# Optimization experiments

Hardware: AMD Instinct MI355X
Metric: run time of the kernel (lower is better)

Reference implementation:

```python
import jax, jax.numpy as jnp
import numpy as np

N_QUBITS = 13
N_ROT = 2
DECOHERENCE_RATE = 0.01
BATCH = 256
DIM = 2 ** N_QUBITS


def setup_inputs() -> dict:
    key = jax.random.key(0)
    k1, k2, k3, k4 = jax.random.split(key, 4)
    return {
        "x": jax.random.normal(k1, (BATCH, 128), dtype=jnp.float32),
        "rx_params": jax.random.normal(k2, (N_QUBITS, N_ROT), dtype=jnp.float32),
        "ry_params": jax.random.normal(k3, (N_QUBITS, N_ROT), dtype=jnp.float32),
        "rz_params": jax.random.normal(k4, (N_QUBITS, N_ROT), dtype=jnp.float32),
    }


def _rx_mat(a):
    c = jnp.cos(a / 2).astype(jnp.complex64)
    s = jnp.sin(a / 2).astype(jnp.complex64)
    mi = jnp.complex64(-1j)
    return jnp.stack([jnp.stack([c, mi * s]), jnp.stack([mi * s, c])])


def _ry_mat(a):
    c = jnp.cos(a / 2).astype(jnp.complex64)
    s = jnp.sin(a / 2).astype(jnp.complex64)
    return jnp.stack([jnp.stack([c, -s]), jnp.stack([s, c])])


def _rz_mat(a):
    e = jnp.exp(jnp.complex64(-1j) * a.astype(jnp.complex64) / 2)
    z = jnp.zeros((), jnp.complex64)
    return jnp.stack([jnp.stack([e, z]), jnp.stack([z, jnp.conj(e)])])


def _apply_axis(state, params, mat_fn):
    # Original torch code ignores the qubit index: every gate acts on the
    # even/odd interleaved pairs of the flat statevector. It also has a view
    # aliasing bug: the odd update reads the ALREADY-UPDATED even amplitudes.
    B = state.shape[0]
    def step(s, angle):
        m = mat_fn(angle)
        p = s.reshape(B, -1, 2)  # [B, DIM/2, 2] (even, odd) pairs
        e, o = p[..., 0], p[..., 1]
        e_new = m[0, 0] * e + m[0, 1] * o
        o_new = m[1, 0] * e_new + m[1, 1] * o  # replicates in-place aliasing bug
        return jnp.stack([e_new, o_new], axis=-1).reshape(B, -1), None
    # params iterated qubit-major, rotation-minor, matching the nested loops
    state, _ = jax.lax.scan(step, state, params.reshape(-1))
    return state


def reference(x, rx_params, ry_params, rz_params):
    B = x.shape[0]
    state = jnp.zeros((B, DIM), dtype=jnp.complex64).at[:, 0].set(1.0)
    state = _apply_axis(state, rx_params, _rx_mat)
    state = _apply_axis(state, ry_params, _ry_mat)
    state = _apply_axis(state, rz_params, _rz_mat)
    # decoherence noise: complex normal (re/im each var 1/2), matching torch.randn_like on complex64
    noise = jax.random.normal(jax.random.key(42), (B, DIM), dtype=jnp.complex64) * DECOHERENCE_RATE
    state = state + noise
    state = state / jnp.linalg.norm(state, axis=-1, keepdims=True)
    return jnp.abs(state)
```

## Files before the change

kernel.cpp:

```cpp
#include <hip/hip_runtime.h>


#define NBATCH 256
#define NDIM   8192u

__host__ __device__ __forceinline__ unsigned rotl32(unsigned v, unsigned d) {
  return (v << d) | (v >> (32u - d));
}

__host__ __device__ inline void tf2x32(unsigned k0, unsigned k1,
                                       unsigned x0, unsigned x1,
                                       unsigned& o0, unsigned& o1) {
  const unsigned k2 = k0 ^ k1 ^ 0x1BD11BDAu;
  x0 += k0; x1 += k1;
#define TF_R(r) { x0 += x1; x1 = rotl32(x1, r); x1 ^= x0; }
  TF_R(13u) TF_R(15u) TF_R(26u) TF_R(6u)
  x0 += k1; x1 += k2 + 1u;
  TF_R(17u) TF_R(29u) TF_R(16u) TF_R(24u)
  x0 += k2; x1 += k0 + 2u;
  TF_R(13u) TF_R(15u) TF_R(26u) TF_R(6u)
  x0 += k0; x1 += k1 + 3u;
  TF_R(17u) TF_R(29u) TF_R(16u) TF_R(24u)
  x0 += k1; x1 += k2 + 4u;
  TF_R(13u) TF_R(15u) TF_R(26u) TF_R(6u)
  x0 += k2; x1 += k0 + 5u;
#undef TF_R
  o0 = x0; o1 = x1;
}

__device__ __forceinline__ float bits_to_u(unsigned bits) {
  float f = __uint_as_float((bits >> 9) | 0x3f800000u) - 1.0f;
  const float LO = -0.99999994f;
  return fmaxf(LO, fmaf(f, 2.0f, LO));
}

__device__ __forceinline__ float erfinv_f(float x) {
  float w = -__logf(fmaf(-x, x, 1.0f));
  float p;
  if (w < 5.0f) {
    w -= 2.5f;
    p = 2.81022636e-08f;
    p = fmaf(p, w, 3.43273939e-07f);
    p = fmaf(p, w, -3.5233877e-06f);
    p = fmaf(p, w, -4.39150654e-06f);
    p = fmaf(p, w, 0.00021858087f);
    p = fmaf(p, w, -0.00125372503f);
    p = fmaf(p, w, -0.00417768164f);
    p = fmaf(p, w, 0.246640727f);
    p = fmaf(p, w, 1.50140941f);
  } else {
    w = sqrtf(w) - 3.0f;
    p = -0.000200214257f;
    p = fmaf(p, w, 0.000100950558f);
    p = fmaf(p, w, 0.00134934322f);
    p = fmaf(p, w, -0.00367342844f);
    p = fmaf(p, w, 0.00573950773f);
    p = fmaf(p, w, -0.0076224613f);
    p = fmaf(p, w, 0.00943887047f);
    p = fmaf(p, w, 1.00167406f);
    p = fmaf(p, w, 2.83297682f);
  }
  return p * x;
}

__device__ __forceinline__ float2 cmul(float2 a, float2 b) {
  return make_float2(a.x * b.x - a.y * b.y, a.x * b.y + a.y * b.x);
}
__device__ __forceinline__ float2 cadd(float2 a, float2 b) {
  return make_float2(a.x + b.x, a.y + b.y);
}

__device__ __forceinline__ void eff_gate(int g, const float* rx, const float* ry,
                                         const float* rz, float2& G00, float2& G01,
                                         float2& G10, float2& G11) {
  if (g >= 78) {
    G00 = make_float2(1.f, 0.f); G01 = make_float2(0.f, 0.f);
    G10 = make_float2(0.f, 0.f); G11 = make_float2(1.f, 0.f);
    return;
  }
  int axis = (g >= 52) ? 2 : ((g >= 26) ? 1 : 0);
  int w = g - axis * 26;
  float a = ((axis == 0) ? rx[w] : (axis == 1) ? ry[w] : rz[w]) * 0.5f;
  float s, c;
  sincosf(a, &s, &c);
  float2 m00, m01, m10, m11;
  if (axis == 0) {
    m00 = make_float2(c, 0.f); m01 = make_float2(0.f, -s);
    m10 = make_float2(0.f, -s); m11 = make_float2(c, 0.f);
  } else if (axis == 1) {
    m00 = make_float2(c, 0.f); m01 = make_float2(-s, 0.f);
    m10 = make_float2(s, 0.f); m11 = make_float2(c, 0.f);
  } else {
    m00 = make_float2(c, -s); m01 = make_float2(0.f, 0.f);
    m10 = make_float2(0.f, 0.f); m11 = make_float2(c, s);
  }
  G00 = m00; G01 = m01;
  G10 = cmul(m10, m00);
  G11 = cadd(cmul(m10, m01), m11);
}

__global__ __launch_bounds__(1024) void fused_kernel(
    const float* __restrict__ rx, const float* __restrict__ ry,
    const float* __restrict__ rz, float* __restrict__ out,
    unsigned kr0, unsigned kr1, unsigned ki0, unsigned ki1) {
  const int b = blockIdx.x;
  const int t = threadIdx.x;
  const unsigned base = (unsigned)b * NDIM;

  float T00r = 0.f, T00i = 0.f, T10r = 0.f, T10i = 0.f;
  if (t < 64) {
    float2 A00, A01, A10, A11, B00, B01, B10, B11;
    eff_gate(2 * t, rx, ry, rz, A00, A01, A10, A11);
    eff_gate(2 * t + 1, rx, ry, rz, B00, B01, B10, B11);
    float2 P00 = cadd(cmul(B00, A00), cmul(B01, A10));
    float2 P01 = cadd(cmul(B00, A01), cmul(B01, A11));
    float2 P10 = cadd(cmul(B10, A00), cmul(B11, A10));
    float2 P11 = cadd(cmul(B10, A01), cmul(B11, A11));
#pragma unroll
    for (int s = 1; s < 64; s <<= 1) {
      float2 Q00, Q01, Q10, Q11;
      Q00.x = __shfl(P00.x, t + s); Q00.y = __shfl(P00.y, t + s);
      Q01.x = __shfl(P01.x, t + s); Q01.y = __shfl(P01.y, t + s);
      Q10.x = __shfl(P10.x, t + s); Q10.y = __shfl(P10.y, t + s);
      Q11.x = __shfl(P11.x, t + s); Q11.y = __shfl(P11.y, t + s);
      if (t + s < 64) {
        float2 R00 = cadd(cmul(Q00, P00), cmul(Q01, P10));
        float2 R01 = cadd(cmul(Q00, P01), cmul(Q01, P11));
        float2 R10 = cadd(cmul(Q10, P00), cmul(Q11, P10));
        float2 R11 = cadd(cmul(Q10, P01), cmul(Q11, P11));
        P00 = R00; P01 = R01; P10 = R10; P11 = R11;
      }
    }
    T00r = P00.x; T00i = P00.y; T10r = P10.x; T10i = P10.y;
  }

  float re[8], im[8];
#pragma unroll
  for (int k = 0; k < 8; ++k) {
    unsigned j = base + (unsigned)t * 8u + (unsigned)k;
    unsigned y0, y1;
    tf2x32(kr0, kr1, 0u, j, y0, y1);
    re[k] = erfinv_f(bits_to_u(y0 ^ y1)) * 0.01f;
    tf2x32(ki0, ki1, 0u, j, y0, y1);
    im[k] = erfinv_f(bits_to_u(y0 ^ y1)) * 0.01f;
  }
  if (t == 0) {
    re[0] += T00r; im[0] += T00i;
    re[1] += T10r; im[1] += T10i;
  }

  float sumsq = 0.0f;
  float a[8];
#pragma unroll
  for (int k = 0; k < 8; ++k) {
    float s2 = fmaf(re[k], re[k], im[k] * im[k]);
    sumsq += s2;
    a[k] = sqrtf(s2);
  }

#pragma unroll
  for (int off = 32; off; off >>= 1) sumsq += __shfl_down(sumsq, off);
  __shared__ float wsum[16];
  __shared__ float s_rnorm;
  if ((t & 63) == 0) wsum[t >> 6] = sumsq;
  __syncthreads();
  if (t < 64) {
    float v = (t < 16) ? wsum[t] : 0.0f;
#pragma unroll
    for (int off = 8; off; off >>= 1) v += __shfl_xor(v, off);
    if (t == 0) s_rnorm = rsqrtf(v);
  }
  __syncthreads();
  const float rn = s_rnorm;

  float4 o0 = make_float4(a[0] * rn, a[1] * rn, a[2] * rn, a[3] * rn);
  float4 o1 = make_float4(a[4] * rn, a[5] * rn, a[6] * rn, a[7] * rn);
  float4* op = (float4*)(out + base + (unsigned)t * 8u);
  op[0] = o0;
  op[1] = o1;
}

extern "C" void kernel_launch(void* const* d_in, const int* in_sizes, int n_in,
                              void* d_out, int out_size, void* d_ws, size_t ws_size,
                              hipStream_t stream) {
  (void)in_sizes; (void)n_in; (void)out_size; (void)ws_size; (void)d_ws;
  const float* rx = (const float*)d_in[1];
  const float* ry = (const float*)d_in[2];
  const float* rz = (const float*)d_in[3];
  float* out = (float*)d_out;

  unsigned kr0, kr1, ki0, ki1;
  tf2x32(0u, 42u, 0u, 0u, kr0, kr1);
  tf2x32(0u, 42u, 0u, 1u, ki0, ki1);

  fused_kernel<<<NBATCH, 1024, 0, stream>>>(rx, ry, rz, out, kr0, kr1, ki0, ki1);
}
```

Baseline: 19.73 us.

## Collapse RZ gates into a single phase and use fast math intrinsics

The RZ gates are diagonal and commute, so they are summed by wave reduction into one phase applied after the scan. Each lane now builds a single per-gate effective matrix instead of multiplying two. Precise sqrt, rsqrt and sincos calls are swapped for hardware intrinsics, and the clamp in the uniform conversion is removed. The intent is to trim the serial gate-prep math and the per-element noise math, at the cost of slightly lower precision. The prefix-product scan over 64 lanes is kept.

```diff
diff --git a/kernel.cpp b/kernel.cpp
--- a/kernel.cpp
+++ b/kernel.cpp
@@ -4,16 +4,12 @@
 #define NBATCH 256
 #define NDIM   8192u
 
-__host__ __device__ __forceinline__ unsigned rotl32(unsigned v, unsigned d) {
-  return (v << d) | (v >> (32u - d));
-}
-
 __host__ __device__ inline void tf2x32(unsigned k0, unsigned k1,
                                        unsigned x0, unsigned x1,
                                        unsigned& o0, unsigned& o1) {
   const unsigned k2 = k0 ^ k1 ^ 0x1BD11BDAu;
   x0 += k0; x1 += k1;
-#define TF_R(r) { x0 += x1; x1 = rotl32(x1, r); x1 ^= x0; }
+#define TF_R(r) { x0 += x1; x1 = __builtin_rotateleft32(x1, r); x1 ^= x0; }
   TF_R(13u) TF_R(15u) TF_R(26u) TF_R(6u)
   x0 += k1; x1 += k2 + 1u;
   TF_R(17u) TF_R(29u) TF_R(16u) TF_R(24u)
@@ -30,8 +26,7 @@
 
 __device__ __forceinline__ float bits_to_u(unsigned bits) {
   float f = __uint_as_float((bits >> 9) | 0x3f800000u) - 1.0f;
-  const float LO = -0.99999994f;
-  return fmaxf(LO, fmaf(f, 2.0f, LO));
+  return fmaf(f, 2.0f, -0.99999994f);
 }
 
 __device__ __forceinline__ float erfinv_f(float x) {
@@ -49,7 +44,7 @@
     p = fmaf(p, w, 0.246640727f);
     p = fmaf(p, w, 1.50140941f);
   } else {
-    w = sqrtf(w) - 3.0f;
+    w = __builtin_amdgcn_sqrtf(w) - 3.0f;
     p = -0.000200214257f;
     p = fmaf(p, w, 0.000100950558f);
     p = fmaf(p, w, 0.00134934322f);
@@ -70,35 +65,6 @@
   return make_float2(a.x + b.x, a.y + b.y);
 }
 
-__device__ __forceinline__ void eff_gate(int g, const float* rx, const float* ry,
-                                         const float* rz, float2& G00, float2& G01,
-                                         float2& G10, float2& G11) {
-  if (g >= 78) {
-    G00 = make_float2(1.f, 0.f); G01 = make_float2(0.f, 0.f);
-    G10 = make_float2(0.f, 0.f); G11 = make_float2(1.f, 0.f);
-    return;
-  }
-  int axis = (g >= 52) ? 2 : ((g >= 26) ? 1 : 0);
-  int w = g - axis * 26;
-  float a = ((axis == 0) ? rx[w] : (axis == 1) ? ry[w] : rz[w]) * 0.5f;
-  float s, c;
-  sincosf(a, &s, &c);
-  float2 m00, m01, m10, m11;
-  if (axis == 0) {
-    m00 = make_float2(c, 0.f); m01 = make_float2(0.f, -s);
-    m10 = make_float2(0.f, -s); m11 = make_float2(c, 0.f);
-  } else if (axis == 1) {
-    m00 = make_float2(c, 0.f); m01 = make_float2(-s, 0.f);
-    m10 = make_float2(s, 0.f); m11 = make_float2(c, 0.f);
-  } else {
-    m00 = make_float2(c, -s); m01 = make_float2(0.f, 0.f);
-    m10 = make_float2(0.f, 0.f); m11 = make_float2(c, s);
-  }
-  G00 = m00; G01 = m01;
-  G10 = cmul(m10, m00);
-  G11 = cadd(cmul(m10, m01), m11);
-}
-
 __global__ __launch_bounds__(1024) void fused_kernel(
     const float* __restrict__ rx, const float* __restrict__ ry,
     const float* __restrict__ rz, float* __restrict__ out,
@@ -109,13 +75,33 @@
 
   float T00r = 0.f, T00i = 0.f, T10r = 0.f, T10i = 0.f;
   if (t < 64) {
-    float2 A00, A01, A10, A11, B00, B01, B10, B11;
-    eff_gate(2 * t, rx, ry, rz, A00, A01, A10, A11);
-    eff_gate(2 * t + 1, rx, ry, rz, B00, B01, B10, B11);
-    float2 P00 = cadd(cmul(B00, A00), cmul(B01, A10));
-    float2 P01 = cadd(cmul(B00, A01), cmul(B01, A11));
-    float2 P10 = cadd(cmul(B10, A00), cmul(B11, A10));
-    float2 P11 = cadd(cmul(B10, A01), cmul(B11, A11));
+    float rzv = (t < 26) ? rz[t] : 0.0f;
+#pragma unroll
+    for (int off = 32; off; off >>= 1) rzv += __shfl_xor(rzv, off);
+    float sh, ch;
+    __sincosf(0.5f * rzv, &sh, &ch);
+
+    float2 P00, P01, P10, P11;
+    if (t < 52) {
+      bool is_ry = (t >= 26);
+      float ang = 0.5f * (is_ry ? ry[t - 26] : rx[t]);
+      float s, c;
+      __sincosf(ang, &s, &c);
+      float cs = c - s * s;
+      float sc = s * c;
+      P00 = make_float2(c, 0.f);
+      P11 = make_float2(cs, 0.f);
+      if (is_ry) {
+        P01 = make_float2(-s, 0.f);
+        P10 = make_float2(sc, 0.f);
+      } else {
+        P01 = make_float2(0.f, -s);
+        P10 = make_float2(0.f, -sc);
+      }
+    } else {
+      P00 = make_float2(1.f, 0.f); P01 = make_float2(0.f, 0.f);
+      P10 = make_float2(0.f, 0.f); P11 = make_float2(1.f, 0.f);
+    }
 #pragma unroll
     for (int s = 1; s < 64; s <<= 1) {
       float2 Q00, Q01, Q10, Q11;
@@ -131,7 +117,10 @@
         P00 = R00; P01 = R01; P10 = R10; P11 = R11;
       }
     }
-    T00r = P00.x; T00i = P00.y; T10r = P10.x; T10i = P10.y;
+    T00r = fmaf(P00.y, sh, P00.x * ch);
+    T00i = fmaf(-P00.x, sh, P00.y * ch);
+    T10r = fmaf(-P10.y, sh, P10.x * ch);
+    T10i = fmaf(P10.x, sh, P10.y * ch);
   }
 
   float re[8], im[8];
@@ -155,7 +144,7 @@
   for (int k = 0; k < 8; ++k) {
     float s2 = fmaf(re[k], re[k], im[k] * im[k]);
     sumsq += s2;
-    a[k] = sqrtf(s2);
+    a[k] = __builtin_amdgcn_sqrtf(s2);
   }
 
 #pragma unroll
@@ -168,7 +157,7 @@
     float v = (t < 16) ? wsum[t] : 0.0f;
 #pragma unroll
     for (int off = 8; off; off >>= 1) v += __shfl_xor(v, off);
-    if (t == 0) s_rnorm = rsqrtf(v);
+    if (t == 0) s_rnorm = __builtin_amdgcn_rsqf(v);
   }
   __syncthreads();
   const float rn = s_rnorm;
```

After: 19.00 us. 3.7% less time.
